# Kernel tuning notes

Hardware: AMD Instinct MI355X
Metric: run time of the kernel (lower is better)

The kernel has to match this reference:

```python
import jax, jax.numpy as jnp
import numpy as np

L_MAX = 3
H = 32                      # hidden_channels
NI = (L_MAX + 1) ** 2       # 16 irrep components
NELEM = 89
# map each of the 16 irrep components to its l (path index): l=0(1), l=1(3), l=2(5), l=3(7)
L_IDX = np.concatenate([np.full(2 * l + 1, l) for l in range(L_MAX + 1)])


def real_sh_l3(u):
    """Real spherical harmonics up to l=3 on unit vectors u: [E,3] -> [E,16]."""
    x, y, z = u[:, 0], u[:, 1], u[:, 2]
    x2, y2, z2 = x * x, y * y, z * z
    cols = [
        jnp.full_like(x, 0.28209479177387814),                 # l=0
        0.4886025119029199 * y,                                # l=1, m=-1
        0.4886025119029199 * z,                                # l=1, m=0
        0.4886025119029199 * x,                                # l=1, m=1
        1.0925484305920792 * x * y,                            # l=2, m=-2
        1.0925484305920792 * y * z,                            # l=2, m=-1
        0.31539156525252005 * (3.0 * z2 - 1.0),                # l=2, m=0 (|u|=1)
        1.0925484305920792 * x * z,                            # l=2, m=1
        0.5462742152960396 * (x2 - y2),                        # l=2, m=2
        0.5900435899266435 * y * (3.0 * x2 - y2),              # l=3, m=-3
        2.890611442640554 * x * y * z,                         # l=3, m=-2
        0.4570457994644658 * y * (5.0 * z2 - 1.0),             # l=3, m=-1
        0.3731763325901154 * z * (5.0 * z2 - 3.0),             # l=3, m=0
        0.4570457994644658 * x * (5.0 * z2 - 1.0),             # l=3, m=1
        1.445305721320277 * z * (x2 - y2),                     # l=3, m=2
        0.5900435899266435 * x * (x2 - 3.0 * y2),              # l=3, m=3
    ]
    return jnp.stack(cols, axis=-1)


def setup_inputs() -> dict:
    key = jax.random.key(0)
    ks = jax.random.split(key, 12)
    N, E, BOX = 20000, 250000, 30.0
    D = H * NI  # 512
    positions = jax.random.uniform(ks[0], (N, 3), dtype=jnp.float32) * BOX
    cell = jnp.eye(3, dtype=jnp.float32) * BOX
    atomic_numbers = jax.random.randint(ks[1], (N,), 0, NELEM)
    edge_index = jax.random.randint(ks[2], (2, E), 0, N)
    embedding = jax.random.normal(ks[3], (NELEM, D), dtype=jnp.float32) * 0.02
    tp_w0 = jax.random.normal(ks[4], (L_MAX + 1, H, H), dtype=jnp.float32) * 0.01
    tp_w1 = jax.random.normal(ks[5], (L_MAX + 1, H, H), dtype=jnp.float32) * 0.01
    lin_w0 = jax.random.normal(ks[6], (D, D), dtype=jnp.float32) * 0.02
    lin_b0 = jnp.zeros((D,), dtype=jnp.float32)
    lin_w1 = jax.random.normal(ks[7], (D, D), dtype=jnp.float32) * 0.02
    lin_b1 = jnp.zeros((D,), dtype=jnp.float32)
    out_w = jax.random.normal(ks[8], (D, 1), dtype=jnp.float32) * 0.02
    out_b = jnp.zeros((1,), dtype=jnp.float32)
    return dict(positions=positions, cell=cell, atomic_numbers=atomic_numbers,
                edge_index=edge_index, embedding=embedding,
                tp_w0=tp_w0, lin_w0=lin_w0, lin_b0=lin_b0,
                tp_w1=tp_w1, lin_w1=lin_w1, lin_b1=lin_b1,
                out_w=out_w, out_b=out_b)


def _interaction(node_features, src, dst, edge_vectors, tp_w, lin_w, lin_b, N):
    E = edge_vectors.shape[0]
    lengths = jnp.maximum(jnp.linalg.norm(edge_vectors, axis=-1, keepdims=True), 1e-8)
    Y = real_sh_l3(edge_vectors / lengths)              # [E, 16]
    node_src = node_features[src]                       # gather [E, H, 16]
    Wm = tp_w[L_IDX]                                    # [16, H, H] per-irrep channel mix
    msg = jnp.einsum('ecm,mcd->edm', node_src * Y[:, None, :], Wm)  # [E, H, 16]
    agg = jax.ops.segment_sum(msg.reshape(E, -1), dst, num_segments=N)  # [N, H*16]
    out = agg @ lin_w + lin_b
    return out.reshape(N, H, NI)


def reference(positions, cell, atomic_numbers, edge_index, embedding,
              tp_w0, lin_w0, lin_b0, tp_w1, lin_w1, lin_b1, out_w, out_b):
    N = positions.shape[0]
    src, dst = edge_index[0], edge_index[1]
    ev = positions[dst] - positions[src]
    cd = jnp.diagonal(cell)
    ev = ev - jnp.round(ev / cd) * cd                   # minimum-image wrap
    nf = embedding[atomic_numbers].reshape(N, H, NI)
    nf = nf + _interaction(nf, src, dst, ev, tp_w0, lin_w0, lin_b0, N)
    nf = nf + _interaction(nf, src, dst, ev, tp_w1, lin_w1, lin_b1, N)
    node_energies = nf.reshape(N, -1) @ out_w + out_b   # [N, 1]
    return jnp.sum(node_energies)
```

## Files before the change

### kernel.cpp

```cpp
#include <hip/hip_runtime.h>
#include <math.h>

#define DF 512
#define NEMAX 89
#define TPAD 264
#define T1PAD 17

typedef __attribute__((ext_vector_type(8))) unsigned short ushort8;

__device__ __constant__ int c_lidx[16] = {0,1,1,1,2,2,2,2,2,3,3,3,3,3,3,3};

__device__ inline float bf2f(unsigned short s) {
    union { unsigned int u; float f; } x;
    x.u = ((unsigned int)s) << 16;
    return x.f;
}
__device__ inline unsigned short f2bf(float f) {
    union { float f; unsigned int u; } x; x.f = f;
    unsigned int r = x.u + 0x7fffu + ((x.u >> 16) & 1u);
    return (unsigned short)(r >> 16);
}

__device__ inline void sh_eval(float x, float y, float z, float* o)
{
    float x2 = x*x, y2 = y*y, z2 = z*z;
    o[0]  = 0.28209479177387814f;
    o[1]  = 0.4886025119029199f*y;
    o[2]  = 0.4886025119029199f*z;
    o[3]  = 0.4886025119029199f*x;
    o[4]  = 1.0925484305920792f*x*y;
    o[5]  = 1.0925484305920792f*y*z;
    o[6]  = 0.31539156525252005f*(3.0f*z2 - 1.0f);
    o[7]  = 1.0925484305920792f*x*z;
    o[8]  = 0.5462742152960396f*(x2 - y2);
    o[9]  = 0.5900435899266435f*y*(3.0f*x2 - y2);
    o[10] = 2.890611442640554f*x*y*z;
    o[11] = 0.4570457994644658f*y*(5.0f*z2 - 1.0f);
    o[12] = 0.3731763325901154f*z*(5.0f*z2 - 3.0f);
    o[13] = 0.4570457994644658f*x*(5.0f*z2 - 1.0f);
    o[14] = 1.445305721320277f*z*(x2 - y2);
    o[15] = 0.5900435899266435f*x*(x2 - 3.0f*y2);
}

__device__ inline void edge_dir(const float* __restrict__ pos, int s, int d,
                                float cx, float cy, float cz,
                                float& x, float& y, float& z)
{
    float ex = pos[d*3+0] - pos[s*3+0];
    float ey = pos[d*3+1] - pos[s*3+1];
    float ez = pos[d*3+2] - pos[s*3+2];
    ex -= rintf(ex/cx)*cx;
    ey -= rintf(ey/cy)*cy;
    ez -= rintf(ez/cz)*cz;
    float len = fmaxf(sqrtf(ex*ex + ey*ey + ez*ez), 1e-8f);
    x = ex/len; y = ey/len; z = ez/len;
}

__global__ __launch_bounds__(512) void k_setup(const float* __restrict__ lw1,
                                               const float* __restrict__ lw0,
                                               const float* __restrict__ ow,
                                               const float* __restrict__ emb,
                                               const float* __restrict__ tw0,
                                               float* __restrict__ vtmp,
                                               float* __restrict__ wv0,
                                               float* __restrict__ tfe,
                                               uint4* __restrict__ yacc4, int nyacc4,
                                               float* __restrict__ out, int NE)
{
    int b = blockIdx.x, t = threadIdx.x;
    if (b < 128) {
        const float* w = (b < 64) ? lw1 : lw0;
        float* v = (b < 64) ? vtmp : wv0;
        int bb = b & 63;
        int r = bb*8 + (t >> 6);
        int lane = t & 63;
        const float* row = w + (size_t)r * DF;
        float s = 0.0f;
        #pragma unroll
        for (int j = 0; j < 8; j++) s += row[lane + j*64] * ow[lane + j*64];
        #pragma unroll
        for (int off = 32; off > 0; off >>= 1) s += __shfl_xor(s, off, 64);
        if (lane == 0) v[r] = s;
    } else if (b < 128 + NE) {
        __shared__ float nf[DF];
        __shared__ float w[4*32*32];
        int a = b - 128;
        nf[t] = emb[(size_t)a*DF + t];
        for (int i = t; i < 4096; i += 512) w[i] = tw0[i];
        __syncthreads();
        int d = t >> 4, m = t & 15;
        int l = c_lidx[m];
        const float* wl = &w[l*1024 + d];
        float acc = 0.0f;
        #pragma unroll
        for (int c = 0; c < 32; c++) acc += nf[c*16 + m] * wl[c*32];
        tfe[(size_t)a*DF + t] = acc;
    } else {
        int i = (b - 128 - NE)*512 + t;
        if (i < nyacc4) yacc4[i] = make_uint4(0,0,0,0);
        if (i == 0) out[0] = 0.0f;
    }
}

__global__ __launch_bounds__(512) void k_pre2(const float* __restrict__ tw1,
                                              const float* __restrict__ lb1,
                                              const float* __restrict__ lb0,
                                              const float* __restrict__ ow,
                                              const float* __restrict__ ob,
                                              const float* __restrict__ v,
                                              float* __restrict__ u1,
                                              float* __restrict__ hb,
                                              float* __restrict__ out, int N)
{
    __shared__ float vs[DF];
    __shared__ float red[DF];
    __shared__ float us[DF];
    int t = threadIdx.x;
    vs[t] = v[t];
    red[t] = (lb1[t] + lb0[t]) * ow[t];
    __syncthreads();
    int c = t >> 4, m = t & 15, l = c_lidx[m];
    float u = 0.0f;
    #pragma unroll
    for (int d = 0; d < 32; d++) u += tw1[l*1024 + c*32 + d] * vs[d*16 + m];
    u1[t] = u;
    us[t] = u;
    __syncthreads();
    for (int s = 256; s > 0; s >>= 1) {
        if (t < s) red[t] += red[t + s];
        __syncthreads();
    }
    if (t < 16) {
        float s = 0.0f;
        #pragma unroll
        for (int cc = 0; cc < 32; cc++) s += lb0[cc*16 + t] * us[cc*16 + t];
        hb[t] = s;
    }
    if (t == 0) atomicAdd(out, (float)N * (red[0] + ob[0]));
}

__global__ __launch_bounds__(256) void k_gt_helem(const float* __restrict__ lw0,
                                                  const float* __restrict__ u1,
                                                  const float* __restrict__ emb,
                                                  const float* __restrict__ ow,
                                                  const float* __restrict__ hb,
                                                  float* __restrict__ Gt,
                                                  float* __restrict__ hf,
                                                  float* __restrict__ embdot)
{
    int b = blockIdx.x, t = threadIdx.x;
    if (b < 32) {
        int g = b*256 + t;
        int k = g >> 4, m = g & 15;
        float s = 0.0f;
        #pragma unroll
        for (int c = 0; c < 32; c++) s += lw0[(size_t)k*DF + c*16 + m] * u1[c*16 + m];
        Gt[m*DF + k] = s;
    } else {
        __shared__ float r1[256];
        __shared__ float r2[DF];
        int a = b - 32;
        float e0 = emb[(size_t)a*DF + t];
        float e1 = emb[(size_t)a*DF + t + 256];
        r1[t] = e0*ow[t] + e1*ow[t+256];
        r2[t] = e0*u1[t];
        r2[t+256] = e1*u1[t+256];
        __syncthreads();
        for (int s = 128; s > 0; s >>= 1) {
            if (t < s) r1[t] += r1[t + s];
            __syncthreads();
        }
        if (t < 16) {
            float s = hb[t];
            #pragma unroll
            for (int c = 0; c < 32; c++) s += r2[c*16 + t];
            hf[(size_t)a*16 + t] = s;
        }
        if (t == 0) embdot[a] = r1[0];
    }
}

__global__ __launch_bounds__(256) void k_T(const float* __restrict__ tfe,
                                           const float* __restrict__ Gt,
                                           const float* __restrict__ wv0,
                                           unsigned short* __restrict__ Tbf,
                                           float* __restrict__ t1)
{
    __shared__ float tf_s[DF];
    int a = blockIdx.x, t = threadIdx.x;
    tf_s[t]       = tfe[(size_t)a*DF + t];
    tf_s[t + 256] = tfe[(size_t)a*DF + t + 256];
    __syncthreads();
    int mm = t >> 4, m = t & 15;
    float s = 0.0f;
    #pragma unroll
    for (int d = 0; d < 32; d++) s = fmaf(tf_s[d*16 + mm], Gt[m*DF + d*16 + mm], s);
    Tbf[(size_t)a*256 + mm*16 + m] = f2bf(s);
    if (t < 16) {
        float s1 = 0.0f;
        #pragma unroll
        for (int d = 0; d < 32; d++) s1 = fmaf(tf_s[d*16 + t], wv0[d*16 + t], s1);
        t1[(size_t)a*16 + t] = s1;
    }
}

__global__ __launch_bounds__(256) void k_sh_yacc(const float* __restrict__ pos,
                                                 const int* __restrict__ src,
                                                 const int* __restrict__ dst,
                                                 const float* __restrict__ cell,
                                                 float* __restrict__ yacc, int E)
{
    __shared__ float Yl[256][17];
    __shared__ int sAl[256];
    int b = blockIdx.x, t = threadIdx.x;
    int e = b*256 + t;
    float cx = cell[0], cy = cell[4], cz = cell[8];
    if (e < E) {
        int s = src[e], d = dst[e];
        float x, y, z;
        edge_dir(pos, s, d, cx, cy, cz, x, y, z);
        float o[16];
        sh_eval(x, y, z, o);
        #pragma unroll
        for (int j = 0; j < 16; j++) Yl[t][j] = o[j];
        sAl[t] = s;
    }
    __syncthreads();
    int lastvalid = min(256, E - b*256);
    #pragma unroll
    for (int j = 0; j < 16; j++) {
        int idx = j*256 + t;
        int el = idx >> 4, m = idx & 15;
        if (el < lastvalid)
            atomicAdd(&yacc[(size_t)sAl[el]*16 + m], Yl[el][m]);
    }
}

__global__ __launch_bounds__(256) void k_energy(const float* __restrict__ pos,
                                                const int* __restrict__ src,
                                                const int* __restrict__ dst,
                                                const int* __restrict__ an,
                                                const float* __restrict__ cell,
                                                const float* __restrict__ yacc,
                                                const unsigned short* __restrict__ Tbf,
                                                const float* __restrict__ t1,
                                                const float* __restrict__ hf,
                                                const float* __restrict__ embdot,
                                                float* __restrict__ out,
                                                int E, int N, int NE)
{
    __shared__ __align__(16) unsigned short Ts[NEMAX * TPAD];
    __shared__ float t1s[NEMAX * T1PAD];
    __shared__ float wred[4];
    int t = threadIdx.x;
    int nchunk = NE * 32;
    for (int c = t; c < nchunk; c += 256) {
        int a = c >> 5, k = c & 31;
        *(ushort8*)&Ts[a*TPAD + k*8] = *(const ushort8*)&Tbf[(size_t)a*256 + k*8];
    }
    for (int i = t; i < NE*16; i += 256) {
        int a = i >> 4, mm = i & 15;
        t1s[a*T1PAD + mm] = t1[i];
    }
    __syncthreads();

    int i = blockIdx.x * 256 + t;
    float s = 0.0f;
    if (i < E) {
        int sn = src[i], d = dst[i];
        int a = an[sn];
        float x, y, z;
        edge_dir(pos, sn, d, cell[0], cell[4], cell[8], x, y, z);
        float ov[16];
        sh_eval(x, y, z, ov);
        const float4* dp = (const float4*)(yacc + (size_t)d*16);
        float4 D0 = dp[0], D1 = dp[1], D2 = dp[2], D3 = dp[3];
        const unsigned short* Ta = &Ts[a * TPAD];
        const float* ta1 = &t1s[a * T1PAD];
        #pragma unroll
        for (int mm = 0; mm < 16; mm++) {
            ushort8 p0 = *(const ushort8*)&Ta[mm*16];
            ushort8 p1 = *(const ushort8*)&Ta[mm*16 + 8];
            float dotv = bf2f(p0[0])*D0.x + bf2f(p0[1])*D0.y + bf2f(p0[2])*D0.z + bf2f(p0[3])*D0.w
                       + bf2f(p0[4])*D1.x + bf2f(p0[5])*D1.y + bf2f(p0[6])*D1.z + bf2f(p0[7])*D1.w
                       + bf2f(p1[0])*D2.x + bf2f(p1[1])*D2.y + bf2f(p1[2])*D2.z + bf2f(p1[3])*D2.w
                       + bf2f(p1[4])*D3.x + bf2f(p1[5])*D3.y + bf2f(p1[6])*D3.z + bf2f(p1[7])*D3.w;
            s = fmaf(ov[mm], dotv + ta1[mm], s);
        }
    } else if (i < E + N) {
        int n = i - E;
        int a = an[n];
        const float4* hp = (const float4*)(hf + (size_t)a*16);
        float4 H0 = hp[0], H1 = hp[1], H2 = hp[2], H3 = hp[3];
        const float4* vp = (const float4*)(yacc + (size_t)n*16);
        float4 V0 = vp[0], V1 = vp[1], V2 = vp[2], V3 = vp[3];
        s = embdot[a]
          + H0.x*V0.x + H0.y*V0.y + H0.z*V0.z + H0.w*V0.w
          + H1.x*V1.x + H1.y*V1.y + H1.z*V1.z + H1.w*V1.w
          + H2.x*V2.x + H2.y*V2.y + H2.z*V2.z + H2.w*V2.w
          + H3.x*V3.x + H3.y*V3.y + H3.z*V3.z + H3.w*V3.w;
    }
    #pragma unroll
    for (int off = 32; off > 0; off >>= 1) s += __shfl_xor(s, off, 64);
    int lane = t & 63, w = t >> 6;
    if (lane == 0) wred[w] = s;
    __syncthreads();
    if (t == 0) atomicAdd(out, wred[0] + wred[1] + wred[2] + wred[3]);
}

extern "C" void kernel_launch(void* const* d_in, const int* in_sizes, int n_in,
                              void* d_out, int out_size, void* d_ws, size_t ws_size,
                              hipStream_t stream)
{
    const float* pos  = (const float*)d_in[0];
    const float* cell = (const float*)d_in[1];
    const int*   an   = (const int*)d_in[2];
    const int*   ei   = (const int*)d_in[3];
    const float* emb  = (const float*)d_in[4];
    const float* tw0  = (const float*)d_in[5];
    const float* lw0  = (const float*)d_in[6];
    const float* lb0  = (const float*)d_in[7];
    const float* tw1  = (const float*)d_in[8];
    const float* lw1  = (const float*)d_in[9];
    const float* lb1  = (const float*)d_in[10];
    const float* ow   = (const float*)d_in[11];
    const float* ob   = (const float*)d_in[12];
    int N  = in_sizes[0] / 3;
    int E  = in_sizes[3] / 2;
    int NE = in_sizes[4] / DF;
    const int* src = ei;
    const int* dst = ei + E;

    char* ws = (char*)d_ws;
    size_t off = 0;
    auto alloc = [&](size_t bytes) { void* p = ws + off; off += (bytes + 255) / 256 * 256; return p; };

    float* tfe    = (float*)alloc((size_t)NE * DF * 4);
    float* u1     = (float*)alloc(DF * 4);
    float* vtmp   = (float*)alloc(DF * 4);
    float* wv0    = (float*)alloc(DF * 4);
    float* hb     = (float*)alloc(16 * 4);
    float* Gt     = (float*)alloc(16 * DF * 4);
    unsigned short* Tbf = (unsigned short*)alloc((size_t)NE * 256 * 2);
    float* t1     = (float*)alloc((size_t)NE * 16 * 4);
    float* hf     = (float*)alloc((size_t)NE * 16 * 4);
    float* embdot = (float*)alloc((size_t)NE * 4);
    float* yacc   = (float*)alloc((size_t)N * 16 * 4);

    float* out = (float*)d_out;

    int nyacc4 = (N * 64) / 16;
    int zblocks = (nyacc4 + 511) / 512;
    k_setup<<<128 + NE + zblocks, 512, 0, stream>>>(
        lw1, lw0, ow, emb, tw0, vtmp, wv0, tfe, (uint4*)yacc, nyacc4, out, NE);
    k_pre2<<<1, 512, 0, stream>>>(tw1, lb1, lb0, ow, ob, vtmp, u1, hb, out, N);
    k_gt_helem<<<32 + NE, 256, 0, stream>>>(lw0, u1, emb, ow, hb, Gt, hf, embdot);
    k_T<<<NE, 256, 0, stream>>>(tfe, Gt, wv0, Tbf, t1);
    k_sh_yacc<<<(E + 255) / 256, 256, 0, stream>>>(pos, src, dst, cell, yacc, E);
    k_energy<<<(E + N + 255) / 256, 256, 0, stream>>>(
        pos, src, dst, an, cell, yacc, Tbf, t1, hf, embdot, out, E, N, NE);
}
```

Baseline: 60.11 us.

## Fuse mid-stage kernels into one launch with per-block redundant u1 and G compute

Four kernels (k_pre2, k_gt_helem, k_T, k_sh_yacc) are merged into a single k_mid launch whose blocks are partitioned by role: edge spherical-harmonic scatter, bias reduction, per-element T computation and per-element hf/embdot. Each element block recomputes u1, and T blocks also recompute the full 16x512 G matrix into padded shared memory, so the serial dependency chain between small kernels disappears. The hb bias term is folded into hf by adding lb0 to the embedding. The aim is to remove launch gaps and tail serialization. The cost is redundant work: every one of the 89 T blocks reads all of lw0 (1 MB), and the single launch now needs a large shared-memory footprint of about 36 KB per block.

```diff
diff --git a/kernel.cpp b/kernel.cpp
--- a/kernel.cpp
+++ b/kernel.cpp
@@ -5,6 +5,7 @@
 #define NEMAX 89
 #define TPAD 264
 #define T1PAD 17
+#define GP 513
 
 typedef __attribute__((ext_vector_type(8))) unsigned short ushort8;
 
@@ -56,6 +57,21 @@
     x = ex/len; y = ey/len; z = ez/len;
 }
 
+__device__ inline void compute_u1(const float* __restrict__ tw1,
+                                  const float* __restrict__ v,
+                                  float* __restrict__ us, int t)
+{
+    #pragma unroll
+    for (int rep = 0; rep < 2; rep++) {
+        int f = t + rep*256;
+        int c = f >> 4, m = f & 15, l = c_lidx[m];
+        float u = 0.0f;
+        #pragma unroll
+        for (int d = 0; d < 32; d++) u = fmaf(tw1[l*1024 + c*32 + d], v[d*16 + m], u);
+        us[f] = u;
+    }
+}
+
 __global__ __launch_bounds__(512) void k_setup(const float* __restrict__ lw1,
                                                const float* __restrict__ lw0,
                                                const float* __restrict__ ow,
@@ -102,137 +118,117 @@
     }
 }
 
-__global__ __launch_bounds__(512) void k_pre2(const float* __restrict__ tw1,
-                                              const float* __restrict__ lb1,
-                                              const float* __restrict__ lb0,
-                                              const float* __restrict__ ow,
-                                              const float* __restrict__ ob,
-                                              const float* __restrict__ v,
-                                              float* __restrict__ u1,
-                                              float* __restrict__ hb,
-                                              float* __restrict__ out, int N)
-{
-    __shared__ float vs[DF];
-    __shared__ float red[DF];
-    __shared__ float us[DF];
-    int t = threadIdx.x;
-    vs[t] = v[t];
-    red[t] = (lb1[t] + lb0[t]) * ow[t];
-    __syncthreads();
-    int c = t >> 4, m = t & 15, l = c_lidx[m];
-    float u = 0.0f;
-    #pragma unroll
-    for (int d = 0; d < 32; d++) u += tw1[l*1024 + c*32 + d] * vs[d*16 + m];
-    u1[t] = u;
-    us[t] = u;
-    __syncthreads();
-    for (int s = 256; s > 0; s >>= 1) {
-        if (t < s) red[t] += red[t + s];
-        __syncthreads();
-    }
-    if (t < 16) {
+__global__ __launch_bounds__(256) void k_mid(const float* __restrict__ pos,
+                                             const int* __restrict__ src,
+                                             const int* __restrict__ dst,
+                                             const float* __restrict__ cell,
+                                             const float* __restrict__ vtmp,
+                                             const float* __restrict__ wv0,
+                                             const float* __restrict__ tw1,
+                                             const float* __restrict__ lw0,
+                                             const float* __restrict__ lb0,
+                                             const float* __restrict__ lb1,
+                                             const float* __restrict__ ow,
+                                             const float* __restrict__ ob,
+                                             const float* __restrict__ emb,
+                                             const float* __restrict__ tfe,
+                                             float* __restrict__ yacc,
+                                             unsigned short* __restrict__ Tbf,
+                                             float* __restrict__ t1,
+                                             float* __restrict__ hf,
+                                             float* __restrict__ embdot,
+                                             float* __restrict__ out,
+                                             int E, int N, int NE, int EB)
+{
+    __shared__ __align__(16) float smem[512 + 512 + 16*GP];
+    int b = blockIdx.x, t = threadIdx.x;
+    if (b < EB) {
+        float* Yl = smem;
+        int* sAl = (int*)(smem + 256*17);
+        int e = b*256 + t;
+        float cx = cell[0], cy = cell[4], cz = cell[8];
+        if (e < E) {
+            int s = src[e], d = dst[e];
+            float x, y, z;
+            edge_dir(pos, s, d, cx, cy, cz, x, y, z);
+            float o[16];
+            sh_eval(x, y, z, o);
+            #pragma unroll
+            for (int j = 0; j < 16; j++) Yl[t*17 + j] = o[j];
+            sAl[t] = s;
+        }
+        __syncthreads();
+        int lastvalid = min(256, E - b*256);
+        #pragma unroll
+        for (int j = 0; j < 16; j++) {
+            int idx = j*256 + t;
+            int el = idx >> 4, m = idx & 15;
+            if (el < lastvalid)
+                atomicAdd(&yacc[(size_t)sAl[el]*16 + m], Yl[el*17 + m]);
+        }
+    } else if (b == EB) {
+        float* red = smem;
+        red[t] = (lb0[t] + lb1[t])*ow[t] + (lb0[t+256] + lb1[t+256])*ow[t+256];
+        __syncthreads();
+        for (int s = 128; s > 0; s >>= 1) {
+            if (t < s) red[t] += red[t + s];
+            __syncthreads();
+        }
+        if (t == 0) atomicAdd(out, (float)N * (red[0] + ob[0]));
+    } else if (b <= EB + NE) {
+        int a = b - EB - 1;
+        float* us = smem;
+        float* tf = smem + 512;
+        float* g  = smem + 1024;
+        compute_u1(tw1, vtmp, us, t);
+        tf[t]       = tfe[(size_t)a*DF + t];
+        tf[t + 256] = tfe[(size_t)a*DF + t + 256];
+        __syncthreads();
+        for (int i = t; i < 16*DF; i += 256) {
+            int k = i >> 4, m = i & 15;
+            float s = 0.0f;
+            #pragma unroll
+            for (int c = 0; c < 32; c++)
+                s = fmaf(lw0[(size_t)k*DF + c*16 + m], us[c*16 + m], s);
+            g[m*GP + k] = s;
+        }
+        __syncthreads();
+        int mm = t >> 4, m = t & 15;
         float s = 0.0f;
         #pragma unroll
-        for (int cc = 0; cc < 32; cc++) s += lb0[cc*16 + t] * us[cc*16 + t];
-        hb[t] = s;
-    }
-    if (t == 0) atomicAdd(out, (float)N * (red[0] + ob[0]));
-}
-
-__global__ __launch_bounds__(256) void k_gt_helem(const float* __restrict__ lw0,
-                                                  const float* __restrict__ u1,
-                                                  const float* __restrict__ emb,
-                                                  const float* __restrict__ ow,
-                                                  const float* __restrict__ hb,
-                                                  float* __restrict__ Gt,
-                                                  float* __restrict__ hf,
-                                                  float* __restrict__ embdot)
-{
-    int b = blockIdx.x, t = threadIdx.x;
-    if (b < 32) {
-        int g = b*256 + t;
-        int k = g >> 4, m = g & 15;
-        float s = 0.0f;
-        #pragma unroll
-        for (int c = 0; c < 32; c++) s += lw0[(size_t)k*DF + c*16 + m] * u1[c*16 + m];
-        Gt[m*DF + k] = s;
+        for (int d = 0; d < 32; d++)
+            s = fmaf(tf[d*16 + mm], g[m*GP + d*16 + mm], s);
+        Tbf[(size_t)a*256 + mm*16 + m] = f2bf(s);
+        if (t < 16) {
+            float s1 = 0.0f;
+            #pragma unroll
+            for (int d = 0; d < 32; d++) s1 = fmaf(tf[d*16 + t], wv0[d*16 + t], s1);
+            t1[(size_t)a*16 + t] = s1;
+        }
     } else {
-        __shared__ float r1[256];
-        __shared__ float r2[DF];
-        int a = b - 32;
+        int a = b - EB - NE - 1;
+        float* us = smem;
+        float* r2 = smem + 512;
+        float* r1 = smem + 1024;
+        compute_u1(tw1, vtmp, us, t);
         float e0 = emb[(size_t)a*DF + t];
         float e1 = emb[(size_t)a*DF + t + 256];
         r1[t] = e0*ow[t] + e1*ow[t+256];
-        r2[t] = e0*u1[t];
-        r2[t+256] = e1*u1[t+256];
+        __syncthreads();
+        r2[t]       = (e0 + lb0[t])       * us[t];
+        r2[t + 256] = (e1 + lb0[t+256])   * us[t+256];
         __syncthreads();
         for (int s = 128; s > 0; s >>= 1) {
             if (t < s) r1[t] += r1[t + s];
             __syncthreads();
         }
         if (t < 16) {
-            float s = hb[t];
+            float s = 0.0f;
             #pragma unroll
             for (int c = 0; c < 32; c++) s += r2[c*16 + t];
             hf[(size_t)a*16 + t] = s;
         }
         if (t == 0) embdot[a] = r1[0];
-    }
-}
-
-__global__ __launch_bounds__(256) void k_T(const float* __restrict__ tfe,
-                                           const float* __restrict__ Gt,
-                                           const float* __restrict__ wv0,
-                                           unsigned short* __restrict__ Tbf,
-                                           float* __restrict__ t1)
-{
-    __shared__ float tf_s[DF];
-    int a = blockIdx.x, t = threadIdx.x;
-    tf_s[t]       = tfe[(size_t)a*DF + t];
-    tf_s[t + 256] = tfe[(size_t)a*DF + t + 256];
-    __syncthreads();
-    int mm = t >> 4, m = t & 15;
-    float s = 0.0f;
-    #pragma unroll
-    for (int d = 0; d < 32; d++) s = fmaf(tf_s[d*16 + mm], Gt[m*DF + d*16 + mm], s);
-    Tbf[(size_t)a*256 + mm*16 + m] = f2bf(s);
-    if (t < 16) {
-        float s1 = 0.0f;
-        #pragma unroll
-        for (int d = 0; d < 32; d++) s1 = fmaf(tf_s[d*16 + t], wv0[d*16 + t], s1);
-        t1[(size_t)a*16 + t] = s1;
-    }
-}
-
-__global__ __launch_bounds__(256) void k_sh_yacc(const float* __restrict__ pos,
-                                                 const int* __restrict__ src,
-                                                 const int* __restrict__ dst,
-                                                 const float* __restrict__ cell,
-                                                 float* __restrict__ yacc, int E)
-{
-    __shared__ float Yl[256][17];
-    __shared__ int sAl[256];
-    int b = blockIdx.x, t = threadIdx.x;
-    int e = b*256 + t;
-    float cx = cell[0], cy = cell[4], cz = cell[8];
-    if (e < E) {
-        int s = src[e], d = dst[e];
-        float x, y, z;
-        edge_dir(pos, s, d, cx, cy, cz, x, y, z);
-        float o[16];
-        sh_eval(x, y, z, o);
-        #pragma unroll
-        for (int j = 0; j < 16; j++) Yl[t][j] = o[j];
-        sAl[t] = s;
-    }
-    __syncthreads();
-    int lastvalid = min(256, E - b*256);
-    #pragma unroll
-    for (int j = 0; j < 16; j++) {
-        int idx = j*256 + t;
-        int el = idx >> 4, m = idx & 15;
-        if (el < lastvalid)
-            atomicAdd(&yacc[(size_t)sAl[el]*16 + m], Yl[el][m]);
     }
 }
 
@@ -336,11 +332,8 @@
     auto alloc = [&](size_t bytes) { void* p = ws + off; off += (bytes + 255) / 256 * 256; return p; };
 
     float* tfe    = (float*)alloc((size_t)NE * DF * 4);
-    float* u1     = (float*)alloc(DF * 4);
     float* vtmp   = (float*)alloc(DF * 4);
     float* wv0    = (float*)alloc(DF * 4);
-    float* hb     = (float*)alloc(16 * 4);
-    float* Gt     = (float*)alloc(16 * DF * 4);
     unsigned short* Tbf = (unsigned short*)alloc((size_t)NE * 256 * 2);
     float* t1     = (float*)alloc((size_t)NE * 16 * 4);
     float* hf     = (float*)alloc((size_t)NE * 16 * 4);
@@ -353,10 +346,12 @@
     int zblocks = (nyacc4 + 511) / 512;
     k_setup<<<128 + NE + zblocks, 512, 0, stream>>>(
         lw1, lw0, ow, emb, tw0, vtmp, wv0, tfe, (uint4*)yacc, nyacc4, out, NE);
-    k_pre2<<<1, 512, 0, stream>>>(tw1, lb1, lb0, ow, ob, vtmp, u1, hb, out, N);
-    k_gt_helem<<<32 + NE, 256, 0, stream>>>(lw0, u1, emb, ow, hb, Gt, hf, embdot);
-    k_T<<<NE, 256, 0, stream>>>(tfe, Gt, wv0, Tbf, t1);
-    k_sh_yacc<<<(E + 255) / 256, 256, 0, stream>>>(pos, src, dst, cell, yacc, E);
+
+    int EB = (E + 255) / 256;
+    k_mid<<<EB + 1 + 2*NE, 256, 0, stream>>>(
+        pos, src, dst, cell, vtmp, wv0, tw1, lw0, lb0, lb1, ow, ob, emb, tfe,
+        yacc, Tbf, t1, hf, embdot, out, E, N, NE, EB);
+
     k_energy<<<(E + N + 255) / 256, 256, 0, stream>>>(
         pos, src, dst, an, cell, yacc, Tbf, t1, hf, embdot, out, E, N, NE);
 }
```

Result: slower. 62.41 us, median of 2 (+3.8%).
